# Performance work log

Measured on AMD Instinct MI355X. Metric: run time of the kernel, lower is better.

## Reference

```python
import math
import jax, jax.numpy as jnp
import numpy as np

L, B, D, Z, H, N = 2048, 8, 1024, 128, 2048, 16
MAXPOS = 2048
LAPLACE_MU, LAPLACE_SIGMA = 0.707107, 0.282095


def setup_inputs() -> dict:
    key = jax.random.key(0)
    ks = jax.random.split(key, 14)
    def rn(k, shp, s=1.0):
        return jax.random.normal(k, shp, dtype=jnp.float32) * s
    return {
        "x": rn(ks[0], (L, B, D)),
        # MultiHeadEMA params (unidirectional: kernel_dim == D)
        "delta": rn(ks[1], (D, N, 1), 0.2),
        "alpha": rn(ks[2], (D, N, 1), 0.2),
        "beta_ema": rn(ks[3], (D, N, 1), 0.02) + 1.0,
        "gamma_ema": rn(ks[4], (D, N)),
        "omega": rn(ks[5], (D,)),
        # projections
        "v_w": rn(ks[6], (D, H), 0.02), "v_b": jnp.zeros((H,), jnp.float32),
        "mx_w": rn(ks[7], (D, Z + H + 2 * D), 0.02),
        "mx_b": jnp.zeros((Z + H + 2 * D,), jnp.float32),
        "h_w": rn(ks[8], (H, D), 0.02), "h_b": jnp.zeros((D,), jnp.float32),
        # q/k affine from shared z
        "qk_gamma": rn(ks[9], (2, Z), 0.1) + 1.0,
        "qk_beta": rn(ks[10], (2, Z), 0.1),
        # simple relative positional bias
        "rel_pos": rn(ks[11], (2 * MAXPOS - 1,), 0.02),
        # prenorm layernorm
        "ln_w": jnp.ones((D,), jnp.float32),
        "ln_b": jnp.zeros((D,), jnp.float32),
    }


def _laplace(x):
    x = (x - LAPLACE_MU) / (LAPLACE_SIGMA * math.sqrt(2.0))
    return 0.5 * (1.0 + jax.lax.erf(x))


def _layer_norm(x, w, b, eps=1e-5):
    mu = jnp.mean(x, axis=-1, keepdims=True)
    var = jnp.mean(jnp.square(x - mu), axis=-1, keepdims=True)
    return (x - mu) * jax.lax.rsqrt(var + eps) * w + b


def _rel_bias(rel_pos, seq_len):
    # SimpleRelativePositionalBias: Toeplitz (L, L) matrix from a 2L-1 vector
    bvec = rel_pos[MAXPOS - seq_len:MAXPOS + seq_len - 1]  # (2L-1,)
    t = jnp.pad(bvec, (0, seq_len))                         # (3L-1,)
    t = jnp.tile(t, seq_len)[:-seq_len].reshape(seq_len, 3 * seq_len - 2)
    r = (2 * seq_len - 1) // 2
    return t[:, r:t.shape[1] - r]                           # (L, L)


def _ema_conv(xn, delta, alpha, beta_ema, gamma_ema, omega, seq_len):
    # xn: (L, B, D) -> silu(EMA(xn) + xn * omega), via FFT convolution
    scale = 1.0 / math.sqrt(N)
    p = jax.nn.sigmoid(delta)                 # (D, N, 1)
    q = 1.0 - p * jax.nn.sigmoid(alpha)       # (D, N, 1)
    vander = jnp.arange(seq_len, dtype=jnp.float32)[None, None, :] * jnp.log(q)  # (D, N, L)
    kernel = jnp.einsum('dnl,dn->dl', p * beta_ema * jnp.exp(vander), gamma_ema * scale)  # (D, L)
    residual = xn * omega                     # (L, B, D)
    xt = jnp.transpose(xn, (1, 2, 0))         # (B, D, L)
    nfft = 2 * seq_len
    kf = jnp.fft.rfft(kernel, n=nfft)         # (D, L+1) complex
    xf = jnp.fft.rfft(xt, n=nfft)             # (B, D, L+1)
    out = jnp.fft.irfft(xf * kf, n=nfft)[..., :seq_len]  # (B, D, L)
    return jax.nn.silu(jnp.transpose(out, (2, 0, 1)) + residual)  # (L, B, D)


def reference(x, delta, alpha, beta_ema, gamma_ema, omega,
              v_w, v_b, mx_w, mx_b, h_w, h_b,
              qk_gamma, qk_beta, rel_pos, ln_w, ln_b):
    seq_len = x.shape[0]
    residual = x
    xn = _layer_norm(x, ln_w, ln_b)                       # prenorm
    v = jax.nn.silu(xn @ v_w + v_b)                        # (L, B, H)
    mx = _ema_conv(xn, delta, alpha, beta_ema, gamma_ema, omega, seq_len)  # (L, B, D)
    base = mx @ mx_w + mx_b                                # (L, B, D+Z+H+D)
    u = jax.nn.sigmoid(base[..., :D])                      # update gate (L, B, D)
    zr = jax.nn.silu(base[..., D:D + Z + H])
    hx = base[..., D + Z + H:]                             # (L, B, D)
    z = zr[..., :Z]                                        # (L, B, Z)
    r = zr[..., Z:]                                        # (L, B, H)
    zqk = z[..., None, :] * qk_gamma + qk_beta             # (L, B, 2, Z)
    q = jnp.transpose(zqk[..., 0, :], (1, 0, 2))           # (B, L, Z)
    k = jnp.transpose(zqk[..., 1, :], (1, 0, 2))           # (B, L, Z)
    vb = jnp.transpose(v, (1, 0, 2))                       # (B, L, H)
    bias = _rel_bias(rel_pos, seq_len)                     # (L, L)
    qk = jnp.einsum('blz,bmz->blm', q, k) / seq_len + bias # (B, L, L)
    attn = _laplace(qk)
    h = jnp.einsum('blm,bmh->blh', attn, vb)               # (B, L, H)
    h = jnp.transpose(h, (1, 0, 2))                        # (L, B, H)
    h = jax.nn.silu(hx + (h * r) @ h_w + h_b)              # (L, B, D)
    out = residual + u * (h - residual)
    return out
```

## Files before the change

kernel.cpp:

```cpp
#include <hip/hip_runtime.h>
#include <hip/hip_bf16.h>
#include <math.h>

typedef unsigned short u16;
typedef unsigned int   u32;
typedef __bf16 bf16x8_t __attribute__((ext_vector_type(8)));
typedef float  f32x4_t  __attribute__((ext_vector_type(4)));

#define DEVI static __device__ __forceinline__

DEVI float bf2f(u16 u){ union{u32 i; float f;} v; v.i = ((u32)u)<<16; return v.f; }
DEVI u16 f2bf(float f){ union{float f; u32 i;} v; v.f = f; u32 i = v.i; i += 0x7fffu + ((i>>16)&1u); return (u16)(i>>16); }
DEVI float sigm(float x){ return 1.0f/(1.0f + __expf(-x)); }
DEVI float silu_(float x){ return x * sigm(x); }

DEVI void gload16(const u16* gsrc, u16* lds){
  __builtin_amdgcn_global_load_lds(
      (const __attribute__((address_space(1))) unsigned int*)gsrc,
      (__attribute__((address_space(3))) unsigned int*)lds, 16, 0, 0);
}

constexpr int L_=2048, B_=8, D_=1024, Z_=128, H_=2048, N_=16;
constexpr int CH_=128, NC_=16;
constexpr int MXN_=4224, MXNP_=4352;

__global__ __launch_bounds__(256) void k_ln(const float* __restrict__ x,
                                            const float* __restrict__ w,
                                            const float* __restrict__ b,
                                            u16* __restrict__ xn){
  int row = blockIdx.x, t = threadIdx.x;
  int l = row >> 3, bb = row & 7;
  const float4* xr = (const float4*)(x + (size_t)row*D_);
  float4 v = xr[t];
  float s  = v.x+v.y+v.z+v.w;
  float sq = v.x*v.x+v.y*v.y+v.z*v.z+v.w*v.w;
  #pragma unroll
  for (int m=1; m<64; m<<=1){ s += __shfl_xor(s, m); sq += __shfl_xor(sq, m); }
  __shared__ float ss[4], sv[4];
  int wv = t>>6;
  if ((t&63)==0){ ss[wv]=s; sv[wv]=sq; }
  __syncthreads();
  s = ss[0]+ss[1]+ss[2]+ss[3]; sq = sv[0]+sv[1]+sv[2]+sv[3];
  float mu = s*(1.0f/D_);
  float var = sq*(1.0f/D_) - mu*mu;
  float rs = rsqrtf(var + 1e-5f);
  float4 wv4 = ((const float4*)w)[t];
  float4 bv4 = ((const float4*)b)[t];
  u16 o0 = f2bf((v.x-mu)*rs*wv4.x+bv4.x);
  u16 o1 = f2bf((v.y-mu)*rs*wv4.y+bv4.y);
  u16 o2 = f2bf((v.z-mu)*rs*wv4.z+bv4.z);
  u16 o3 = f2bf((v.w-mu)*rs*wv4.w+bv4.w);
  *(uint2*)(xn + ((size_t)bb*L_ + l)*D_ + t*4) =
      make_uint2((u32)o0 | ((u32)o1<<16), (u32)o2 | ((u32)o3<<16));
}

__global__ __launch_bounds__(256) void k_tr(const float* __restrict__ in, int R, int C,
                                            u16* __restrict__ out){
  __shared__ u16 TT[32*33];
  int c0 = blockIdx.x*32, r0 = blockIdx.y*32;
  int t = threadIdx.x;
  int lr = t>>3, lc4 = (t&7)*4;
  float4 v = *(const float4*)&in[(size_t)(r0+lr)*C + c0 + lc4];
  TT[(lc4+0)*33 + lr] = f2bf(v.x);
  TT[(lc4+1)*33 + lr] = f2bf(v.y);
  TT[(lc4+2)*33 + lr] = f2bf(v.z);
  TT[(lc4+3)*33 + lr] = f2bf(v.w);
  __syncthreads();
  int orr = t>>3, oc4 = (t&7)*4;
  u16 a0 = TT[orr*33 + oc4+0], a1 = TT[orr*33 + oc4+1];
  u16 a2 = TT[orr*33 + oc4+2], a3 = TT[orr*33 + oc4+3];
  *(uint2*)&out[(size_t)(c0+orr)*R + r0 + oc4] =
      make_uint2((u32)a0 | ((u32)a1<<16), (u32)a2 | ((u32)a3<<16));
}

__global__ void k_ema_params(const float* __restrict__ delta, const float* __restrict__ alpha,
                             const float* __restrict__ beta,  const float* __restrict__ gamma,
                             float* __restrict__ qA, float* __restrict__ wcA, float* __restrict__ qPA){
  int i = blockIdx.x*256 + threadIdx.x;
  if (i >= D_*N_) return;
  float p = 1.0f/(1.0f + expf(-delta[i]));
  float q = 1.0f - p*(1.0f/(1.0f + expf(-alpha[i])));
  qA[i]  = q;
  wcA[i] = p*beta[i]*gamma[i]*0.25f;
  qPA[i] = powf(q, (float)CH_);
}

__global__ __launch_bounds__(256) void k_ema_a(const u16* __restrict__ xn,
                                               const float* __restrict__ qA,
                                               float* __restrict__ F){
  int d = blockIdx.x*256 + threadIdx.x;
  int b = blockIdx.y, c = blockIdx.z;
  float q[N_], s[N_];
  #pragma unroll
  for (int n=0;n<N_;n++){ q[n]=qA[d*N_+n]; s[n]=0.0f; }
  for (int t=0;t<CH_;t++){
    int l = c*CH_ + t;
    float x = bf2f(xn[((size_t)b*L_ + l)*D_ + d]);
    #pragma unroll
    for (int n=0;n<N_;n++) s[n] = q[n]*s[n] + x;
  }
  float* Fo = F + (((size_t)c*B_ + b)*D_ + d)*N_;
  #pragma unroll
  for (int n=0;n<N_;n++) Fo[n] = s[n];
}

__global__ __launch_bounds__(256) void k_ema_b(float* __restrict__ F,
                                               const float* __restrict__ qPA){
  int i = blockIdx.x*256 + threadIdx.x;
  int n = i & (N_-1);
  int d = (i>>4) & (D_-1);
  int b = i >> 14;
  float qP = qPA[d*N_+n];
  float S = 0.0f;
  for (int c=0;c<NC_;c++){
    size_t idx = (((size_t)c*B_ + b)*D_ + d)*N_ + n;
    float f = F[idx];
    F[idx] = S;
    S = qP*S + f;
  }
}

__global__ __launch_bounds__(256) void k_ema_c(const u16* __restrict__ xn,
                                               const float* __restrict__ qA,
                                               const float* __restrict__ wcA,
                                               const float* __restrict__ CY,
                                               const float* __restrict__ omega,
                                               u16* __restrict__ mx){
  int d = blockIdx.x*256 + threadIdx.x;
  int b = blockIdx.y, c = blockIdx.z;
  float q[N_], wc[N_], s[N_];
  const float* cy = CY + (((size_t)c*B_ + b)*D_ + d)*N_;
  #pragma unroll
  for (int n=0;n<N_;n++){ q[n]=qA[d*N_+n]; wc[n]=wcA[d*N_+n]; s[n]=cy[n]; }
  float om = omega[d];
  for (int t=0;t<CH_;t++){
    int l = c*CH_ + t;
    float x = bf2f(xn[((size_t)b*L_ + l)*D_ + d]);
    float acc = 0.0f;
    #pragma unroll
    for (int n=0;n<N_;n++){ s[n] = q[n]*s[n] + x; acc += wc[n]*s[n]; }
    mx[((size_t)b*L_ + l)*D_ + d] = f2bf(silu_(acc + x*om));
  }
}

template<int OP>
DEVI void epi_store(int row0, int col, f32x4_t v4,
                    u16* Cb, int ldc,
                    u16* P0b, u16* P1b, u16* P2b, u16* P3b,
                    const u16* RP0b,
                    const float* biasC, const float* biasR,
                    const float* qkg, const float* qkb){
  #pragma unroll
  for (int r2=0;r2<4;r2++){
    int row = row0 + r2;
    float v = v4[r2];
    if (OP == 0) {
      Cb[(size_t)row*ldc + col] = f2bf(silu_(v + biasR[row]));
    } else if (OP == 1) {
      if (col < MXN_) {
        v += biasC[col];
        if (col < 1024) {
          P0b[(size_t)row*1024 + col] = f2bf(sigm(v));
        } else if (col < 1152) {
          float s = silu_(v);
          int zi = col - 1024;
          P2b[(size_t)row*128 + zi] = f2bf(s*qkg[zi]     + qkb[zi]);
          P3b[(size_t)row*128 + zi] = f2bf(s*qkg[128+zi] + qkb[128+zi]);
        } else if (col < 3200) {
          Cb[(size_t)row*2048 + (col-1152)] = f2bf(silu_(v));
        } else {
          P1b[(size_t)row*1024 + (col-3200)] = f2bf(v);
        }
      }
    } else {
      v *= bf2f(RP0b[(size_t)row*ldc + col]);
      Cb[(size_t)row*ldc + col] = f2bf(v);
    }
  }
}

#define ACC_LIST(X) \
  X(0,0) X(0,1) X(0,2) X(0,3)  X(1,0) X(1,1) X(1,2) X(1,3) \
  X(2,0) X(2,1) X(2,2) X(2,3)  X(3,0) X(3,1) X(3,2) X(3,3) \
  X(4,0) X(4,1) X(4,2) X(4,3)  X(5,0) X(5,1) X(5,2) X(5,3) \
  X(6,0) X(6,1) X(6,2) X(6,3)  X(7,0) X(7,1) X(7,2) X(7,3)
#define AF_LIST(X) X(0) X(1) X(2) X(3) X(4) X(5) X(6) X(7)
#define BF_LIST(X) X(0) X(1) X(2) X(3)

#define DECL_ACC(M,N) f32x4_t A_##M##_##N = (f32x4_t){0.f,0.f,0.f,0.f};
#define MFMA_STEP(M,N) A_##M##_##N = __builtin_amdgcn_mfma_f32_16x16x32_bf16(AF##M, BF##N, A_##M##_##N, 0,0,0);
#define LD_AF(M) bf16x8_t AF##M = *(const bf16x8_t*)&LDS[_ab + (wr*128 + M*16 + lane15)*64 + kfx];
#define LD_BF(N) bf16x8_t BF##N = *(const bf16x8_t*)&LDS[_ab + 16384 + (wc*64 + N*16 + lane15)*64 + kfx];
#define EPI_ST(M,N) epi_store<OP>(rowBase + wr*128 + M*16 + lane4*4, \
                                  colBase + wc*64 + N*16 + lane15, A_##M##_##N, \
                                  Cb, ldc, P0b, P1b, P2b, P3b, RP0b, biasC, biasR, qkg, qkb);

#define STG8(BUF, K0) do {                                                        \
    int _ab = (BUF)*32768;                                                        \
    _Pragma("unroll")                                                             \
    for (int it=0; it<4; ++it){                                                   \
      int idx = it*512 + tid; int r = idx>>3, ch = idx&7;                         \
      gload16(Ab + (size_t)(rowBase + r)*lda + (K0) + ((ch ^ (r&7))*8),           \
              &LDS[_ab + idx*8]);                                                 \
    }                                                                             \
    _Pragma("unroll")                                                             \
    for (int it=0; it<4; ++it){                                                   \
      int idx = it*512 + tid; int r = idx>>3, ch = idx&7;                         \
      gload16(Bb + (size_t)(colBase + r)*ldb + (K0) + ((ch ^ (r&7))*8),           \
              &LDS[_ab + 16384 + idx*8]);                                         \
    }                                                                             \
  } while(0)

#define CMP8(BUF) do {                                                            \
    int _ab = (BUF)*32768;                                                        \
    int _sw = (lane15&7)<<3;                                                      \
    { int kfx = (lane4*8) ^ _sw;                                                  \
      AF_LIST(LD_AF)  BF_LIST(LD_BF)                                              \
      __builtin_amdgcn_s_setprio(1);                                              \
      ACC_LIST(MFMA_STEP)                                                         \
      __builtin_amdgcn_s_setprio(0);                                              \
    }                                                                             \
    { int kfx = (32 + lane4*8) ^ _sw;                                             \
      AF_LIST(LD_AF)  BF_LIST(LD_BF)                                              \
      __builtin_amdgcn_s_setprio(1);                                              \
      ACC_LIST(MFMA_STEP)                                                         \
      __builtin_amdgcn_s_setprio(0);                                              \
    }                                                                             \
  } while(0)

template<int OP>
__global__ __launch_bounds__(512, 2) void k_g8(
    const u16* __restrict__ A, int lda, long aStr,
    const u16* __restrict__ Bm, int ldb, long bStr,
    int K,
    u16* __restrict__ C, int ldc, long cStr,
    const float* __restrict__ biasC, const float* __restrict__ biasR,
    const float* __restrict__ qkg, const float* __restrict__ qkb,
    u16* __restrict__ P0, u16* __restrict__ P1,
    u16* __restrict__ P2, u16* __restrict__ P3,
    const u16* __restrict__ RP0)
{
  __shared__ u16 LDS[65536];
  int zz = blockIdx.z;
  const u16* Ab = A + (size_t)zz*aStr;
  const u16* Bb = Bm + (size_t)zz*bStr;

  int gx = gridDim.x;
  int f = blockIdx.x + gx*blockIdx.y;
  int q8 = (gx*gridDim.y) >> 3;
  int wg = (f & 7)*q8 + (f >> 3);
  int rowBase = (wg / gx)*256;
  int colBase = (wg % gx)*256;

  int tid = threadIdx.x;
  int lane = tid & 63, wave = tid >> 6;
  int wr = wave >> 2, wc = wave & 3;
  int lane15 = lane & 15, lane4 = lane >> 4;

  ACC_LIST(DECL_ACC)

  int nt = K >> 6;
  STG8(0, 0);
  STG8(1, 64);
  for (int t = 0; t < nt; ++t){
    if (t + 1 < nt) { asm volatile("s_waitcnt vmcnt(8)" ::: "memory"); }
    else            { asm volatile("s_waitcnt vmcnt(0)" ::: "memory"); }
    __builtin_amdgcn_s_barrier();
    __builtin_amdgcn_sched_barrier(0);
    CMP8(t & 1);
    if (t + 2 < nt) {
      __builtin_amdgcn_s_barrier();
      STG8(t & 1, (t+2)*64);
    }
  }

  u16* Cb  = C  ? C  + (size_t)zz*cStr : nullptr;
  u16* P0b = P0 ? P0 + (size_t)zz*((size_t)L_*D_) : nullptr;
  u16* P1b = P1 ? P1 + (size_t)zz*((size_t)L_*D_) : nullptr;
  u16* P2b = P2 ? P2 + (size_t)zz*((size_t)L_*Z_) : nullptr;
  u16* P3b = P3 ? P3 + (size_t)zz*((size_t)L_*Z_) : nullptr;
  const u16* RP0b = RP0 ? RP0 + (size_t)zz*((size_t)L_*H_) : nullptr;

  ACC_LIST(EPI_ST)
}

#define STG(BUF, K0) do {                                                         \
    int _ab = (BUF)*16384;                                                        \
    _Pragma("unroll")                                                             \
    for (int it=0; it<4; ++it){                                                   \
      int idx = it*256 + tid; int r = idx>>3, ch = idx&7;                         \
      gload16(Ab + (size_t)(rowBase + r)*lda + (K0) + ((ch ^ (r&7))*8),           \
              &LDS[_ab + idx*8]);                                                 \
    }                                                                             \
    _Pragma("unroll")                                                             \
    for (int it=0; it<4; ++it){                                                   \
      int idx = it*256 + tid; int r = idx>>3, ch = idx&7;                         \
      gload16(Bb + (size_t)(colBase + r)*ldb + (K0) + ((ch ^ (r&7))*8),           \
              &LDS[_ab + 8192 + idx*8]);                                          \
    }                                                                             \
  } while(0)

#define CMP(BUF) do {                                                             \
    int _ab = (BUF)*16384;                                                        \
    _Pragma("unroll")                                                             \
    for (int ks=0; ks<2; ++ks){                                                   \
      bf16x8_t af[4], bfr[4];                                                     \
      int kfx = (ks*32 + lane4*8) ^ ((lane15&7)<<3);                              \
      _Pragma("unroll")                                                           \
      for (int m=0;m<4;m++)                                                       \
        af[m]  = *(const bf16x8_t*)&LDS[_ab + (wm + m*16 + lane15)*64 + kfx];     \
      _Pragma("unroll")                                                           \
      for (int n=0;n<4;n++)                                                       \
        bfr[n] = *(const bf16x8_t*)&LDS[_ab + 8192 + (wn + n*16 + lane15)*64 + kfx]; \
      __builtin_amdgcn_s_setprio(1);                                              \
      _Pragma("unroll")                                                           \
      for (int m=0;m<4;m++)                                                       \
        _Pragma("unroll")                                                         \
        for (int n=0;n<4;n++)                                                     \
          acc[m][n] = __builtin_amdgcn_mfma_f32_16x16x32_bf16(af[m], bfr[n], acc[m][n], 0,0,0); \
      __builtin_amdgcn_s_setprio(0);                                              \
    }                                                                             \
  } while(0)

template<int OP>
__global__ __launch_bounds__(256) void k_gall(
    const u16* __restrict__ A, int lda, long aStr,
    const u16* __restrict__ Bm, int ldb, long bStr,
    int K,
    u16* __restrict__ C, int ldc, long cStr,
    const float* __restrict__ biasC,
    const float* __restrict__ relpos,
    const u16* __restrict__ RP0, const u16* __restrict__ RP1,
    const float* __restrict__ xin, float* __restrict__ outf, int bb)
{
  __shared__ u16 LDS[32768];
  int zz = blockIdx.z;
  const u16* Ab = A + (size_t)zz*aStr;
  const u16* Bb = Bm + (size_t)zz*bStr;

  int gx = gridDim.x;
  int f = blockIdx.x + gx*blockIdx.y;
  int q8 = (gx*gridDim.y) >> 3;
  int wg = (f & 7)*q8 + (f >> 3);
  int rowBase = (wg / gx)*128;
  int colBase = (wg % gx)*128;

  int tid = threadIdx.x;
  int lane = tid & 63, wave = tid >> 6;
  int wm = (wave>>1)*64, wn = (wave&1)*64;
  int lane15 = lane & 15, lane4 = lane >> 4;

  f32x4_t acc[4][4];
  #pragma unroll
  for (int m=0;m<4;m++)
    #pragma unroll
    for (int n=0;n<4;n++) acc[m][n] = (f32x4_t){0.f,0.f,0.f,0.f};

  int nt = K >> 6;
  STG(0, 0);
  STG(1, 64);
  for (int t = 0; t < nt; ++t){
    if (t + 1 < nt) { asm volatile("s_waitcnt vmcnt(8)" ::: "memory"); }
    else            { asm volatile("s_waitcnt vmcnt(0)" ::: "memory"); }
    __builtin_amdgcn_s_barrier();
    __builtin_amdgcn_sched_barrier(0);
    CMP(t & 1);
    if (t + 2 < nt) {
      __builtin_amdgcn_s_barrier();
      STG(t & 1, (t+2)*64);
    }
  }

  u16* Cb = C ? C + (size_t)zz*cStr : nullptr;
  const u16* RP0b = RP0 ? RP0 + (size_t)zz*((size_t)L_*D_) : nullptr;
  const u16* RP1b = RP1 ? RP1 + (size_t)zz*((size_t)L_*D_) : nullptr;
  int bglob = bb + zz;

  #pragma unroll
  for (int m=0;m<4;m++) {
    #pragma unroll
    for (int n=0;n<4;n++) {
      int col = colBase + wn + n*16 + lane15;
      #pragma unroll
      for (int r2=0;r2<4;r2++) {
        int row = rowBase + wm + m*16 + lane4*4 + r2;
        float v = acc[m][n][r2];
        if (OP == 2) {
          v = v*(1.0f/(float)L_) + relpos[2047 + col - row];
          v = 0.5f*(1.0f + erff((v - 0.707107f)*2.5066282746f));
          Cb[(size_t)row*ldc + col] = f2bf(v);
        } else {
          v += biasC[col];
          float hx = bf2f(RP0b[(size_t)row*1024 + col]);
          float hval = silu_(hx + v);
          size_t gi = ((size_t)row*B_ + bglob)*D_ + col;
          float xv = xin[gi];
          float uu = bf2f(RP1b[(size_t)row*1024 + col]);
          outf[gi] = xv + uu*(hval - xv);
        }
      }
    }
  }
}

extern "C" void kernel_launch(void* const* d_in, const int* in_sizes, int n_in,
                              void* d_out, int out_size, void* d_ws, size_t ws_size,
                              hipStream_t stream) {
  const float* x      = (const float*)d_in[0];
  const float* delta  = (const float*)d_in[1];
  const float* alpha  = (const float*)d_in[2];
  const float* betaE  = (const float*)d_in[3];
  const float* gammaE = (const float*)d_in[4];
  const float* omega  = (const float*)d_in[5];
  const float* v_w    = (const float*)d_in[6];
  const float* v_b    = (const float*)d_in[7];
  const float* mx_w   = (const float*)d_in[8];
  const float* mx_b   = (const float*)d_in[9];
  const float* h_w    = (const float*)d_in[10];
  const float* h_b    = (const float*)d_in[11];
  const float* qkg    = (const float*)d_in[12];
  const float* qkb    = (const float*)d_in[13];
  const float* relpos = (const float*)d_in[14];
  const float* ln_w   = (const float*)d_in[15];
  const float* ln_b   = (const float*)d_in[16];
  float* out = (float*)d_out;

  const size_t fixedB = 92995584ull;
  const size_t perNB  = 42991616ull;
  int NB = 8;
  while (NB > 1 && fixedB + (size_t)NB*perNB > ws_size) NB >>= 1;
  int NG = B_ / NB;

  char* ws = (char*)d_ws;
  size_t o = 0;
  auto alloc = [&](size_t sz){ size_t r = o; o += sz; return r; };
  u16* XN    = (u16*)(ws + alloc(33554432));
  u16* MX    = (u16*)(ws + alloc(33554432));
  u16* VWT   = (u16*)(ws + alloc(4194304));
  u16* MXWT  = (u16*)(ws + alloc((size_t)MXNP_*D_*2));
  u16* HWT   = (u16*)(ws + alloc(4194304));
  float* EQ  = (float*)(ws + alloc(65536));
  float* EW  = (float*)(ws + alloc(65536));
  float* EP  = (float*)(ws + alloc(65536));
  float* Ff  = (float*)(ws + alloc(8388608));
  u16* VT    = (u16*)(ws + alloc((size_t)NB*8388608));
  u16* ATTN  = (u16*)(ws + alloc((size_t)NB*8388608));
  u16* Rb    = (u16*)(ws + alloc((size_t)NB*8388608));
  u16* HRb   = (u16*)(ws + alloc((size_t)NB*8388608));
  u16* Ub    = (u16*)(ws + alloc((size_t)NB*4194304));
  u16* HXb   = (u16*)(ws + alloc((size_t)NB*4194304));
  u16* Qb    = (u16*)(ws + alloc((size_t)NB*524288));
  u16* Kb    = (u16*)(ws + alloc((size_t)NB*524288));

  k_ln<<<L_*B_, 256, 0, stream>>>(x, ln_w, ln_b, XN);
  k_ema_params<<<(D_*N_+255)/256, 256, 0, stream>>>(delta, alpha, betaE, gammaE, EQ, EW, EP);
  k_ema_a<<<dim3(D_/256, B_, NC_), 256, 0, stream>>>(XN, EQ, Ff);
  k_ema_b<<<(B_*D_*N_)/256, 256, 0, stream>>>(Ff, EP);
  k_ema_c<<<dim3(D_/256, B_, NC_), 256, 0, stream>>>(XN, EQ, EW, Ff, omega, MX);
  k_tr<<<dim3(H_/32, D_/32), 256, 0, stream>>>(v_w, D_, H_, VWT);
  k_tr<<<dim3(MXN_/32, D_/32), 256, 0, stream>>>(mx_w, D_, MXN_, MXWT);
  k_tr<<<dim3(D_/32, H_/32), 256, 0, stream>>>(h_w, H_, D_, HWT);

  for (int g = 0; g < NG; ++g) {
    int b0 = g*NB;
    k_g8<0><<<dim3(L_/256, H_/256, NB), 512, 0, stream>>>(
        VWT, D_, 0L, XN + (size_t)b0*L_*D_, D_, (long)L_*D_, D_,
        VT, L_, (long)H_*L_,
        nullptr, v_b, nullptr, nullptr,
        nullptr, nullptr, nullptr, nullptr, nullptr);
    k_g8<1><<<dim3(MXNP_/256, L_/256, NB), 512, 0, stream>>>(
        MX + (size_t)b0*L_*D_, D_, (long)L_*D_, MXWT, D_, 0L, D_,
        Rb, H_, (long)L_*H_,
        mx_b, nullptr, qkg, qkb,
        Ub, HXb, Qb, Kb, nullptr);
    k_gall<2><<<dim3(L_/128, L_/128, NB), 256, 0, stream>>>(
        Qb, Z_, (long)L_*Z_, Kb, Z_, (long)L_*Z_, Z_,
        ATTN, L_, (long)L_*L_,
        nullptr, relpos, nullptr, nullptr, nullptr, nullptr, 0);
    k_g8<3><<<dim3(H_/256, L_/256, NB), 512, 0, stream>>>(
        ATTN, L_, (long)L_*L_, VT, L_, (long)H_*L_, L_,
        HRb, H_, (long)L_*H_,
        nullptr, nullptr, nullptr, nullptr,
        nullptr, nullptr, nullptr, nullptr, Rb);
    k_gall<4><<<dim3(D_/128, L_/128, NB), 256, 0, stream>>>(
        HRb, H_, (long)L_*H_, HWT, H_, 0L, H_,
        nullptr, 0, 0L,
        h_b, nullptr, HXb, Ub, x, out, b0);
  }
}
```

Before: 810.9 us.

## Interleave half-tile global loads with MFMA phases in 256x256 GEMM

Result: no change. 814.5 us (+0.4%).

```diff
diff --git a/kernel.cpp b/kernel.cpp
--- a/kernel.cpp
+++ b/kernel.cpp
@@ -184,49 +184,72 @@
   X(2,0) X(2,1) X(2,2) X(2,3)  X(3,0) X(3,1) X(3,2) X(3,3) \
   X(4,0) X(4,1) X(4,2) X(4,3)  X(5,0) X(5,1) X(5,2) X(5,3) \
   X(6,0) X(6,1) X(6,2) X(6,3)  X(7,0) X(7,1) X(7,2) X(7,3)
-#define AF_LIST(X) X(0) X(1) X(2) X(3) X(4) X(5) X(6) X(7)
-#define BF_LIST(X) X(0) X(1) X(2) X(3)
-
 #define DECL_ACC(M,N) f32x4_t A_##M##_##N = (f32x4_t){0.f,0.f,0.f,0.f};
-#define MFMA_STEP(M,N) A_##M##_##N = __builtin_amdgcn_mfma_f32_16x16x32_bf16(AF##M, BF##N, A_##M##_##N, 0,0,0);
-#define LD_AF(M) bf16x8_t AF##M = *(const bf16x8_t*)&LDS[_ab + (wr*128 + M*16 + lane15)*64 + kfx];
-#define LD_BF(N) bf16x8_t BF##N = *(const bf16x8_t*)&LDS[_ab + 16384 + (wc*64 + N*16 + lane15)*64 + kfx];
 #define EPI_ST(M,N) epi_store<OP>(rowBase + wr*128 + M*16 + lane4*4, \
                                   colBase + wc*64 + N*16 + lane15, A_##M##_##N, \
                                   Cb, ldc, P0b, P1b, P2b, P3b, RP0b, biasC, biasR, qkg, qkb);
 
-#define STG8(BUF, K0) do {                                                        \
-    int _ab = (BUF)*32768;                                                        \
+#define MFMA_PAIR(M, NA, NB) \
+  A_##M##_##NA = __builtin_amdgcn_mfma_f32_16x16x32_bf16(AF##M, BFa, A_##M##_##NA, 0,0,0); \
+  A_##M##_##NB = __builtin_amdgcn_mfma_f32_16x16x32_bf16(AF##M, BFb, A_##M##_##NB, 0,0,0);
+#define MFMA_PH(NA, NB) \
+  MFMA_PAIR(0,NA,NB) MFMA_PAIR(1,NA,NB) MFMA_PAIR(2,NA,NB) MFMA_PAIR(3,NA,NB) \
+  MFMA_PAIR(4,NA,NB) MFMA_PAIR(5,NA,NB) MFMA_PAIR(6,NA,NB) MFMA_PAIR(7,NA,NB)
+
+#define AF_RD(M) AF##M = *(const bf16x8_t*)&LDS[_ab + wr*8192 + (M*16 + lane15)*64 + kfx];
+#define AF_ALL AF_RD(0) AF_RD(1) AF_RD(2) AF_RD(3) AF_RD(4) AF_RD(5) AF_RD(6) AF_RD(7)
+#define BRD(NN) (*(const bf16x8_t*)&LDS[_ab + 16384 + (wc>>1)*8192 + \
+                 (((wc&1)*64 + NN*16 + lane15)*64) + kfx])
+
+#define STAGE_HALF(DSTU16, SRC, LD, K0) do {                                      \
     _Pragma("unroll")                                                             \
-    for (int it=0; it<4; ++it){                                                   \
+    for (int it=0; it<2; ++it){                                                   \
       int idx = it*512 + tid; int r = idx>>3, ch = idx&7;                         \
-      gload16(Ab + (size_t)(rowBase + r)*lda + (K0) + ((ch ^ (r&7))*8),           \
-              &LDS[_ab + idx*8]);                                                 \
-    }                                                                             \
-    _Pragma("unroll")                                                             \
-    for (int it=0; it<4; ++it){                                                   \
-      int idx = it*512 + tid; int r = idx>>3, ch = idx&7;                         \
-      gload16(Bb + (size_t)(colBase + r)*ldb + (K0) + ((ch ^ (r&7))*8),           \
-              &LDS[_ab + 16384 + idx*8]);                                         \
+      gload16((SRC) + (size_t)r*(LD) + (K0) + ((ch ^ (r&7))*8),                   \
+              &LDS[(DSTU16) + idx*8]);                                            \
     }                                                                             \
   } while(0)
 
-#define CMP8(BUF) do {                                                            \
-    int _ab = (BUF)*32768;                                                        \
-    int _sw = (lane15&7)<<3;                                                      \
-    { int kfx = (lane4*8) ^ _sw;                                                  \
-      AF_LIST(LD_AF)  BF_LIST(LD_BF)                                              \
-      __builtin_amdgcn_s_setprio(1);                                              \
-      ACC_LIST(MFMA_STEP)                                                         \
-      __builtin_amdgcn_s_setprio(0);                                              \
-    }                                                                             \
-    { int kfx = (32 + lane4*8) ^ _sw;                                             \
-      AF_LIST(LD_AF)  BF_LIST(LD_BF)                                              \
-      __builtin_amdgcn_s_setprio(1);                                              \
-      ACC_LIST(MFMA_STEP)                                                         \
-      __builtin_amdgcn_s_setprio(0);                                              \
-    }                                                                             \
-  } while(0)
+#define BARR  __builtin_amdgcn_s_barrier();
+#define LGKM0 asm volatile("s_waitcnt lgkmcnt(0)" ::: "memory"); \
+              __builtin_amdgcn_sched_barrier(0);
+
+#define TILEB(AB, OB) \
+  { const int _ab = (AB); const int _ob = (OB);                                   \
+    bf16x8_t AF0,AF1,AF2,AF3,AF4,AF5,AF6,AF7,BFa,BFb;                             \
+    { int kfx = (lane4*8) ^ sw;                \
+      AF_ALL                                                                      \
+      BFa = BRD(0); BFb = BRD(1);                                                 \
+      if (s1) STAGE_HALF(_ob + 8192, Ab + (size_t)(rowBase+128)*lda, lda, k1);    \
+      BARR LGKM0                                                                  \
+      __builtin_amdgcn_s_setprio(1); MFMA_PH(0,1) __builtin_amdgcn_s_setprio(0);  \
+      BARR                                                                        \
+    }                                                                             \
+    { int kfx = (lane4*8) ^ sw;                \
+      BFa = BRD(2); BFb = BRD(3);                                                 \
+      if (s1) STAGE_HALF(_ob + 16384, Bb + (size_t)colBase*ldb, ldb, k1);         \
+      BARR LGKM0                                                                  \
+      __builtin_amdgcn_s_setprio(1); MFMA_PH(2,3) __builtin_amdgcn_s_setprio(0);  \
+      BARR                                                                        \
+    }                                                                             \
+    { int kfx = (32 + lane4*8) ^ sw;           \
+      AF_ALL                                                                      \
+      BFa = BRD(0); BFb = BRD(1);                                                 \
+      if (s1) STAGE_HALF(_ob + 24576, Bb + (size_t)(colBase+128)*ldb, ldb, k1);   \
+      BARR LGKM0                                                                  \
+      __builtin_amdgcn_s_setprio(1); MFMA_PH(0,1) __builtin_amdgcn_s_setprio(0);  \
+      BARR                                                                        \
+    }                                                                             \
+    { int kfx = (32 + lane4*8) ^ sw;           \
+      BFa = BRD(2); BFb = BRD(3);                                                 \
+      if (s2) STAGE_HALF(_ab + 0, Ab + (size_t)rowBase*lda, lda, k2);             \
+      if (s2)      { asm volatile("s_waitcnt vmcnt(2)" ::: "memory"); }           \
+      else if (s1) { asm volatile("s_waitcnt vmcnt(0)" ::: "memory"); }           \
+      BARR LGKM0                                                                  \
+      __builtin_amdgcn_s_setprio(1); MFMA_PH(2,3) __builtin_amdgcn_s_setprio(0);  \
+      BARR                                                                        \
+    }                                                                             \
+  }
 
 template<int OP>
 __global__ __launch_bounds__(512, 2) void k_g8(
@@ -256,22 +279,24 @@
   int lane = tid & 63, wave = tid >> 6;
   int wr = wave >> 2, wc = wave & 3;
   int lane15 = lane & 15, lane4 = lane >> 4;
+  int sw = (lane15 & 7) << 3;
 
   ACC_LIST(DECL_ACC)
 
   int nt = K >> 6;
-  STG8(0, 0);
-  STG8(1, 64);
-  for (int t = 0; t < nt; ++t){
-    if (t + 1 < nt) { asm volatile("s_waitcnt vmcnt(8)" ::: "memory"); }
-    else            { asm volatile("s_waitcnt vmcnt(0)" ::: "memory"); }
-    __builtin_amdgcn_s_barrier();
-    __builtin_amdgcn_sched_barrier(0);
-    CMP8(t & 1);
-    if (t + 2 < nt) {
-      __builtin_amdgcn_s_barrier();
-      STG8(t & 1, (t+2)*64);
-    }
+  STAGE_HALF(0,      Ab + (size_t)rowBase*lda,        lda, 0);
+  STAGE_HALF(8192,   Ab + (size_t)(rowBase+128)*lda,  lda, 0);
+  STAGE_HALF(16384,  Bb + (size_t)colBase*ldb,        ldb, 0);
+  STAGE_HALF(24576,  Bb + (size_t)(colBase+128)*ldb,  ldb, 0);
+  STAGE_HALF(32768,  Ab + (size_t)rowBase*lda,        lda, 64);
+  asm volatile("s_waitcnt vmcnt(2)" ::: "memory");
+  __builtin_amdgcn_s_barrier();
+
+  for (int t = 0; t < nt; t += 2){
+    { int k1=(t+1)<<6, k2=(t+2)<<6; bool s1=(t+1)<nt, s2=(t+2)<nt;
+      TILEB(0, 32768) }
+    { int k1=(t+2)<<6, k2=(t+3)<<6; bool s1=(t+2)<nt, s2=(t+3)<nt;
+      TILEB(32768, 0) }
   }
 
   u16* Cb  = C  ? C  + (size_t)zz*cStr : nullptr;
```
